# Kernel tuning notes

Hardware: AMD Instinct MI355X
Metric: run time of the kernel (lower is better)

The kernel has to match this reference:

```python
import jax, jax.numpy as jnp
import numpy as np

V, D, S, L, DK, DV, H, B = 32000, 1024, 1024, 4, 64, 64, 16, 4
DFF = 4 * D
EPS = 1e-5


def setup_inputs() -> dict:
    key = jax.random.key(0)
    ks = jax.random.split(key, 20)
    s = 0.02
    n = jax.random.normal
    return {
        "idx": jax.random.randint(ks[0], (B, S), 0, V, dtype=jnp.int32),
        "tok_emb": n(ks[1], (V, D), jnp.float32) * s,
        "pos_emb": n(ks[2], (S, D), jnp.float32) * s,
        "wq": n(ks[3], (L, H, D, DK), jnp.float32) * s,
        "wk": n(ks[4], (L, H, D, DK), jnp.float32) * s,
        "wv": n(ks[5], (L, H, D, DV), jnp.float32) * s,
        "wo": n(ks[6], (L, H * DV, D), jnp.float32) * s,
        "w1": n(ks[7], (L, D, DFF), jnp.float32) * s,
        "b1": jnp.zeros((L, DFF), jnp.float32),
        "w2": n(ks[8], (L, DFF, D), jnp.float32) * s,
        "b2": jnp.zeros((L, D), jnp.float32),
        "ln1_g": jnp.ones((L, D), jnp.float32),
        "ln1_b": jnp.zeros((L, D), jnp.float32),
        "ln2_g": jnp.ones((L, D), jnp.float32),
        "ln2_b": jnp.zeros((L, D), jnp.float32),
        "lnf_g": jnp.ones((D,), jnp.float32),
        "lnf_b": jnp.zeros((D,), jnp.float32),
        "lm_w": n(ks[9], (D, V), jnp.float32) * s,
        "lm_b": jnp.zeros((V,), jnp.float32),
    }


def _ln(x, g, b):
    mu = jnp.mean(x, axis=-1, keepdims=True)
    var = jnp.mean(jnp.square(x - mu), axis=-1, keepdims=True)
    return (x - mu) * jax.lax.rsqrt(var + EPS) * g + b


def _gpt(idx, tok_emb, pos_emb, wq, wk, wv, wo, w1, b1, w2, b2,
         ln1_g, ln1_b, ln2_g, ln2_b, lnf_g, lnf_b, lm_w, lm_b):
    x = tok_emb[idx] + pos_emb[None, :, :]          # [B,S,D]
    causal = jnp.tril(jnp.ones((S, S), bool))        # tril mask buffer
    scale = 1.0 / jnp.sqrt(jnp.asarray(DK, x.dtype))

    def block(x, p):
        wq, wk, wv, wo, w1, b1, w2, b2, g1, be1, g2, be2 = p
        h = _ln(x, g1, be1)
        Q = jnp.einsum('bsd,hdk->bhsk', h, wq)
        K = jnp.einsum('bsd,hdk->bhsk', h, wk)
        Vv = jnp.einsum('bsd,hdv->bhsv', h, wv)
        att = jnp.einsum('bhsk,bhtk->bhst', Q, K) * scale
        att = jnp.where(causal, att, -jnp.inf)
        att = jax.nn.softmax(att, axis=-1)
        o = jnp.einsum('bhst,bhtv->bshv', att, Vv).reshape(x.shape[0], S, H * DV)
        x = x + o @ wo
        h2 = _ln(x, g2, be2)
        x = x + jax.nn.relu(h2 @ w1 + b1) @ w2 + be2 * 0 + b2
        return x, None

    x, _ = jax.lax.scan(block, x, (wq, wk, wv, wo, w1, b1, w2, b2,
                                   ln1_g, ln1_b, ln2_g, ln2_b))
    x = _ln(x, lnf_g, lnf_b)
    logits = x @ lm_w + lm_b                          # [B,S,V]
    return logits


def reference(idx, tok_emb, pos_emb, wq, wk, wv, wo, w1, b1, w2, b2,
              ln1_g, ln1_b, ln2_g, ln2_b, lnf_g, lnf_b, lm_w, lm_b):
    return _gpt(idx, tok_emb, pos_emb, wq, wk, wv, wo, w1, b1, w2, b2,
                ln1_g, ln1_b, ln2_g, ln2_b, lnf_g, lnf_b, lm_w, lm_b)
```

## Files before the change

### kernel.cpp

```cpp
#include <hip/hip_runtime.h>
#include <hip/hip_bf16.h>

#define V_   32000
#define VP_  32768
#define D_   1024
#define S_   1024
#define L_   4
#define H_   16
#define B_   4
#define DFF_ 4096
#define M_   (B_*S_)

using bf_t = __hip_bfloat16;
typedef __bf16 bf16x8 __attribute__((ext_vector_type(8)));
typedef __bf16 bf16x4 __attribute__((ext_vector_type(4)));
typedef float  f32x4  __attribute__((ext_vector_type(4)));

#define AS1(p) ((__attribute__((address_space(1))) void*)(p))
#define AS3(p) ((__attribute__((address_space(3))) void*)(p))

__global__ __launch_bounds__(256) void k_transpose_bf16(
    const float* __restrict__ src, bf_t* __restrict__ dst,
    int R, int C, long srcS1, long srcS2, long dstS1, long dstS2, int n2)
{
  const int z  = blockIdx.z;
  const int z1 = z / n2, z2 = z % n2;
  src += (size_t)z1 * srcS1 + (size_t)z2 * srcS2;
  dst += (size_t)z1 * dstS1 + (size_t)z2 * dstS2;
  __shared__ float tile[32][33];
  const int c0 = blockIdx.x * 32, r0 = blockIdx.y * 32;
  const int lx = threadIdx.x, ly = threadIdx.y;
  #pragma unroll
  for (int i = 0; i < 32; i += 8)
    tile[ly + i][lx] = src[(size_t)(r0 + ly + i) * C + (c0 + lx)];
  __syncthreads();
  #pragma unroll
  for (int i = 0; i < 32; i += 8)
    dst[(size_t)(c0 + ly + i) * R + (r0 + lx)] = __float2bfloat16(tile[lx][ly + i]);
}

__global__ __launch_bounds__(256) void k_embed(
    const int* __restrict__ idx, const float* __restrict__ tok,
    const float* __restrict__ pos, float* __restrict__ x)
{
  const int row = blockIdx.x;
  const int s   = row & (S_ - 1);
  const int t   = idx[row];
  const float4* tr = (const float4*)(tok + (size_t)t * D_);
  const float4* pr = (const float4*)(pos + (size_t)s * D_);
  float4* xr = (float4*)(x + (size_t)row * D_);
  const int i = threadIdx.x;
  float4 a = tr[i], b = pr[i];
  xr[i] = make_float4(a.x + b.x, a.y + b.y, a.z + b.z, a.w + b.w);
}

__global__ __launch_bounds__(256) void k_ln(
    const float* __restrict__ x, const float* __restrict__ g,
    const float* __restrict__ bb, bf_t* __restrict__ out)
{
  __shared__ float red[8];
  const int row = blockIdx.x, tid = threadIdx.x;
  const float4 v = ((const float4*)(x + (size_t)row * D_))[tid];
  float s = v.x + v.y + v.z + v.w;
  #pragma unroll
  for (int o = 32; o > 0; o >>= 1) s += __shfl_down(s, o);
  if ((tid & 63) == 0) red[tid >> 6] = s;
  __syncthreads();
  const float mu = (red[0] + red[1] + red[2] + red[3]) * (1.f / D_);
  const float dx = v.x - mu, dy = v.y - mu, dz = v.z - mu, dw = v.w - mu;
  float ss = dx*dx + dy*dy + dz*dz + dw*dw;
  #pragma unroll
  for (int o = 32; o > 0; o >>= 1) ss += __shfl_down(ss, o);
  if ((tid & 63) == 0) red[4 + (tid >> 6)] = ss;
  __syncthreads();
  const float var = (red[4] + red[5] + red[6] + red[7]) * (1.f / D_);
  const float rs  = rsqrtf(var + 1e-5f);
  const float4 gv = ((const float4*)g)[tid];
  const float4 bv = ((const float4*)bb)[tid];
  const size_t base = (size_t)row * D_ + tid * 4;
  out[base + 0] = __float2bfloat16(dx * rs * gv.x + bv.x);
  out[base + 1] = __float2bfloat16(dy * rs * gv.y + bv.y);
  out[base + 2] = __float2bfloat16(dz * rs * gv.z + bv.z);
  out[base + 3] = __float2bfloat16(dw * rs * gv.w + bv.w);
}

__global__ __launch_bounds__(256) void k_combine_ln(
    float* __restrict__ x, const float* __restrict__ P, long pstride,
    const float* __restrict__ cbias,
    const float* __restrict__ g, const float* __restrict__ bb,
    bf_t* __restrict__ out)
{
  __shared__ float red[8];
  const int row = blockIdx.x, tid = threadIdx.x;
  const size_t i = (size_t)row * 256 + tid;
  float4 a = ((const float4*)x)[i];
  {
    const float4 p0 = ((const float4*)P)[i];
    const float4 p1 = ((const float4*)(P + pstride))[i];
    a.x += p0.x + p1.x; a.y += p0.y + p1.y;
    a.z += p0.z + p1.z; a.w += p0.w + p1.w;
  }
  if (cbias) {
    const float4 bv = ((const float4*)cbias)[tid];
    a.x += bv.x; a.y += bv.y; a.z += bv.z; a.w += bv.w;
  }
  ((float4*)x)[i] = a;
  float s = a.x + a.y + a.z + a.w;
  #pragma unroll
  for (int o = 32; o > 0; o >>= 1) s += __shfl_down(s, o);
  if ((tid & 63) == 0) red[tid >> 6] = s;
  __syncthreads();
  const float mu = (red[0] + red[1] + red[2] + red[3]) * (1.f / D_);
  const float dx = a.x - mu, dy = a.y - mu, dz = a.z - mu, dw = a.w - mu;
  float ss = dx*dx + dy*dy + dz*dz + dw*dw;
  #pragma unroll
  for (int o = 32; o > 0; o >>= 1) ss += __shfl_down(ss, o);
  if ((tid & 63) == 0) red[4 + (tid >> 6)] = ss;
  __syncthreads();
  const float var = (red[4] + red[5] + red[6] + red[7]) * (1.f / D_);
  const float rs  = rsqrtf(var + 1e-5f);
  const float4 gv = ((const float4*)g)[tid];
  const float4 bv = ((const float4*)bb)[tid];
  const size_t base = (size_t)row * D_ + tid * 4;
  out[base + 0] = __float2bfloat16(dx * rs * gv.x + bv.x);
  out[base + 1] = __float2bfloat16(dy * rs * gv.y + bv.y);
  out[base + 2] = __float2bfloat16(dz * rs * gv.z + bv.z);
  out[base + 3] = __float2bfloat16(dw * rs * gv.w + bv.w);
}

template<bool HAS_BIAS, bool RELU, bool OUT_BF16, bool NT, int PARTS>
__global__ __launch_bounds__(256) void k_gemm(
    const bf_t* __restrict__ A, const bf_t* __restrict__ Bt,
    float* outF, bf_t* outB,
    const float* __restrict__ bias,
    int N, int ld, int Klen, long pstride)
{
  __shared__ __bf16 As[128 * 64];
  __shared__ __bf16 Bs[128 * 64];
  const int tid  = threadIdx.x;
  const int lane = tid & 63, wid = tid >> 6;
  int bp = blockIdx.x, kh = 0;
  if (PARTS > 1) { const int T = gridDim.x / PARTS; kh = bp / T; bp %= T; }
  const int i  = bp >> 3;
  const int nt = (bp & 7) + 8 * (i >> 5);
  const int mt = i & 31;
  const int m0 = mt * 128;
  const int n0 = nt * 128;
  if (n0 >= N) return;
  const int kb = kh * Klen;
  f32x4 acc[4][4] = {};

  const int srow = lane >> 3;
  const int scol = (lane & 7) * 8;
  const int mw = (wid >> 1) * 64, nw = (wid & 1) * 64;

  for (int kt = 0; kt < Klen; kt += 64) {
    #pragma unroll
    for (int i2 = 0; i2 < 4; ++i2) {
      const int chunk = i2 * 4 + wid;
      const int r = chunk * 8 + srow;
      const bf_t* sa = A  + (size_t)(m0 + r) * ld + kb + kt + scol;
      const bf_t* sb = Bt + (size_t)(n0 + r) * ld + kb + kt + scol;
      __builtin_amdgcn_global_load_lds(AS1(sa), AS3(&As[chunk * 512]), 16, 0, 0);
      __builtin_amdgcn_global_load_lds(AS1(sb), AS3(&Bs[chunk * 512]), 16, 0, 0);
    }
    asm volatile("s_waitcnt vmcnt(0)" ::: "memory");
    __syncthreads();
    #pragma unroll
    for (int kk = 0; kk < 2; ++kk) {
      bf16x8 af[4], bfr[4];
      #pragma unroll
      for (int mi = 0; mi < 4; ++mi)
        af[mi] = *(const bf16x8*)&As[(mw + mi * 16 + (lane & 15)) * 64 + kk * 32 + (lane >> 4) * 8];
      #pragma unroll
      for (int ni = 0; ni < 4; ++ni)
        bfr[ni] = *(const bf16x8*)&Bs[(nw + ni * 16 + (lane & 15)) * 64 + kk * 32 + (lane >> 4) * 8];
      #pragma unroll
      for (int mi = 0; mi < 4; ++mi)
        #pragma unroll
        for (int ni = 0; ni < 4; ++ni)
          acc[mi][ni] = __builtin_amdgcn_mfma_f32_16x16x32_bf16(af[mi], bfr[ni], acc[mi][ni], 0, 0, 0);
    }
    __syncthreads();
  }

  float* outP = outF + (PARTS > 1 ? (size_t)kh * pstride : 0);
  const int cr = (lane >> 4) * 4, cc = lane & 15;
  #pragma unroll
  for (int mi = 0; mi < 4; ++mi) {
    #pragma unroll
    for (int ni = 0; ni < 4; ++ni) {
      const int col = n0 + nw + ni * 16 + cc;
      const float bv = HAS_BIAS ? bias[col] : 0.f;
      #pragma unroll
      for (int j = 0; j < 4; ++j) {
        const int row = m0 + mw + mi * 16 + cr + j;
        float v = acc[mi][ni][j] + bv;
        if (RELU)  v = fmaxf(v, 0.f);
        if (OUT_BF16) {
          outB[(size_t)row * N + col] = __float2bfloat16(v);
        } else if (NT) {
          __builtin_nontemporal_store(v, &outP[(size_t)row * N + col]);
        } else {
          outP[(size_t)row * N + col] = v;
        }
      }
    }
  }
}

__device__ __forceinline__ void stage256(
    const bf_t* __restrict__ A, const bf_t* __restrict__ Bt,
    int m0, int n0, int lda, int kt, int wid, int lane, __bf16* buf)
{
  #pragma unroll
  for (int p = 0; p < 4; ++p) {
    const int sb   = p * 512 + wid * 64;
    const int slot = sb + lane;
    const int row  = slot >> 3;
    const int c    = (slot & 7) ^ (row & 7);
    __builtin_amdgcn_global_load_lds(AS1(A  + (size_t)(m0 + row) * lda + kt + c * 8),
                                     AS3(buf + sb * 8), 16, 0, 0);
    __builtin_amdgcn_global_load_lds(AS1(Bt + (size_t)(n0 + row) * lda + kt + c * 8),
                                     AS3(buf + 16384 + sb * 8), 16, 0, 0);
  }
}

template<bool HAS_BIAS, bool RELU, bool OUT_BF16, bool NT, int MAP>
__global__ __launch_bounds__(512, 2) void k_gemm256(
    const bf_t* __restrict__ A, const bf_t* __restrict__ Bt,
    float* outF, bf_t* outB, const float* __restrict__ bias,
    int N, int Nvalid, int K)
{
  __shared__ __align__(16) __bf16 LDS[65536];
  const int tid = threadIdx.x, lane = tid & 63, wid = tid >> 6;
  int mt, nt;
  if (MAP == 0) { mt = blockIdx.x & 15; nt = blockIdx.x >> 4; }
  else {
    const int xcd = blockIdx.x & 7, i = blockIdx.x >> 3;
    mt = i & 15; nt = xcd + 8 * (i >> 4);
  }
  const int m0 = mt * 256, n0 = nt * 256;
  if (n0 >= Nvalid) return;
  const int wm = wid >> 2, wn = wid & 3;
  const int l4 = lane & 15, lhi = lane >> 4;

  f32x4 acc[8][4] = {};
  const int NTILES = K >> 6;

  stage256(A, Bt, m0, n0, K, 0,  wid, lane, LDS);
  stage256(A, Bt, m0, n0, K, 64, wid, lane, LDS + 32768);

  for (int t = 0; t < NTILES; ++t) {
    __bf16* buf = LDS + (t & 1) * 32768;
    if (t < NTILES - 1) asm volatile("s_waitcnt vmcnt(8)" ::: "memory");
    else                asm volatile("s_waitcnt vmcnt(0)" ::: "memory");
    __builtin_amdgcn_s_barrier();
    asm volatile("" ::: "memory");
    #pragma unroll
    for (int kk = 0; kk < 2; ++kk) {
      const int ck = kk * 4 + lhi;
      bf16x8 aq[8], bq[4];
      #pragma unroll
      for (int mi = 0; mi < 8; ++mi) {
        const int r = wm * 128 + mi * 16 + l4;
        aq[mi] = *(const bf16x8*)&buf[r * 64 + ((ck ^ (r & 7)) * 8)];
      }
      #pragma unroll
      for (int ni = 0; ni < 4; ++ni) {
        const int r = wn * 64 + ni * 16 + l4;
        bq[ni] = *(const bf16x8*)&buf[16384 + r * 64 + ((ck ^ (r & 7)) * 8)];
      }
      __builtin_amdgcn_s_setprio(1);
      #pragma unroll
      for (int mi = 0; mi < 8; ++mi)
        #pragma unroll
        for (int ni = 0; ni < 4; ++ni)
          acc[mi][ni] = __builtin_amdgcn_mfma_f32_16x16x32_bf16(aq[mi], bq[ni], acc[mi][ni], 0, 0, 0);
      __builtin_amdgcn_s_setprio(0);
    }
    asm volatile("" ::: "memory");
    __builtin_amdgcn_s_barrier();
    if (t + 2 < NTILES)
      stage256(A, Bt, m0, n0, K, (t + 2) * 64, wid, lane, buf);
  }

  float* slab = (float*)LDS + wid * 1088;
  float bval[4];
  if (HAS_BIAS) {
    #pragma unroll
    for (int ni = 0; ni < 4; ++ni) bval[ni] = bias[n0 + wn * 64 + ni * 16 + l4];
  }
  #pragma unroll
  for (int mi = 0; mi < 8; ++mi) {
    #pragma unroll
    for (int ni = 0; ni < 4; ++ni)
      #pragma unroll
      for (int j = 0; j < 4; ++j) {
        float v = acc[mi][ni][j];
        if (HAS_BIAS) v += bval[ni];
        if (RELU) v = fmaxf(v, 0.f);
        slab[(lhi * 4 + j) * 68 + ni * 16 + l4] = v;
      }
    const int grow0 = m0 + wm * 128 + mi * 16;
    const int ncol0 = n0 + wn * 64;
    #pragma unroll
    for (int q = 0; q < 4; ++q) {
      const int r16 = q * 4 + lhi;
      const f32x4 v = *(const f32x4*)&slab[r16 * 68 + l4 * 4];
      const size_t gaddr = (size_t)(grow0 + r16) * N + ncol0 + l4 * 4;
      if (OUT_BF16) {
        bf16x4 o4;
        o4[0] = (__bf16)v[0]; o4[1] = (__bf16)v[1];
        o4[2] = (__bf16)v[2]; o4[3] = (__bf16)v[3];
        *(bf16x4*)(outB + gaddr) = o4;
      } else if (NT) {
        __builtin_nontemporal_store(v, (f32x4*)(outF + gaddr));
      } else {
        *(f32x4*)(outF + gaddr) = v;
      }
    }
  }
}

__global__ __launch_bounds__(256) void k_attn_mfma(
    const bf_t* __restrict__ qkv, bf_t* __restrict__ o)
{
  __shared__ __bf16 Qs[64 * 64];
  __shared__ __bf16 Ks[64 * 64];
  __shared__ __bf16 Vt[64 * 64];
  __shared__ __bf16 Ps[4][16 * 64];

  const int qt = blockIdx.x, bh = blockIdx.y;
  const int b = bh >> 4, h = bh & 15;
  const int tid = threadIdx.x, lane = tid & 63, wid = tid >> 6;
  const int qbase = qt * 64;
  const int r0 = wid * 16;
  const int l4 = lane & 15, lhi = lane >> 4;

  #pragma unroll
  for (int p = 0; p < 2; ++p) {
    const int idx = p * 256 + tid;
    const int r = idx >> 3, c8 = idx & 7;
    const bf16x8 v = *(const bf16x8*)(qkv + (size_t)(b * S_ + qbase + r) * 3072 + h * 64 + c8 * 8);
    *(bf16x8*)&Qs[r * 64 + ((c8 ^ (r & 7)) * 8)] = v;
  }

  f32x4 oa[4];
  #pragma unroll
  for (int di = 0; di < 4; ++di) oa[di] = (f32x4){0.f, 0.f, 0.f, 0.f};
  float mrow = -1e30f, lrow = 0.f;

  const float SCL = 0.125f * 1.44269504089f;

  for (int kt = 0; kt <= qt; ++kt) {
    __syncthreads();
    #pragma unroll
    for (int p = 0; p < 2; ++p) {
      const int idx = p * 256 + tid;
      const int r = idx >> 3, c8 = idx & 7;
      const size_t gbase = (size_t)(b * S_ + kt * 64 + r) * 3072 + h * 64 + c8 * 8;
      const bf16x8 kv = *(const bf16x8*)(qkv + gbase + 1024);
      *(bf16x8*)&Ks[r * 64 + ((c8 ^ (r & 7)) * 8)] = kv;
      const bf16x8 vv = *(const bf16x8*)(qkv + gbase + 2048);
      #pragma unroll
      for (int i = 0; i < 8; ++i) {
        const int d = c8 * 8 + i;
        Vt[d * 64 + (((r >> 3) ^ i ^ c8) * 8) + (r & 7)] = vv[i];
      }
    }
    __syncthreads();

    f32x4 s[4];
    #pragma unroll
    for (int ni = 0; ni < 4; ++ni) s[ni] = (f32x4){0.f, 0.f, 0.f, 0.f};
    const int qr = r0 + l4;
    __builtin_amdgcn_s_setprio(1);
    #pragma unroll
    for (int kk = 0; kk < 2; ++kk) {
      const int ck = kk * 4 + lhi;
      const bf16x8 bq = *(const bf16x8*)&Qs[qr * 64 + ((ck ^ (qr & 7)) * 8)];
      #pragma unroll
      for (int ni = 0; ni < 4; ++ni) {
        const int t = ni * 16 + l4;
        const bf16x8 ak = *(const bf16x8*)&Ks[t * 64 + ((ck ^ (t & 7)) * 8)];
        s[ni] = __builtin_amdgcn_mfma_f32_16x16x32_bf16(ak, bq, s[ni], 0, 0, 0);
      }
    }
    __builtin_amdgcn_s_setprio(0);

    #pragma unroll
    for (int ni = 0; ni < 4; ++ni)
      #pragma unroll
      for (int j = 0; j < 4; ++j)
        s[ni][j] *= SCL;
    if (kt == qt) {
      #pragma unroll
      for (int ni = 0; ni < 4; ++ni)
        #pragma unroll
        for (int j = 0; j < 4; ++j)
          if (ni * 16 + lhi * 4 + j > r0 + l4) s[ni][j] = -1e30f;
    }

    float mloc = -1e30f;
    #pragma unroll
    for (int ni = 0; ni < 4; ++ni)
      #pragma unroll
      for (int j = 0; j < 4; ++j) mloc = fmaxf(mloc, s[ni][j]);
    mloc = fmaxf(mloc, __shfl_xor(mloc, 16));
    mloc = fmaxf(mloc, __shfl_xor(mloc, 32));
    float cscale = 1.f;
    if (!__all(mloc <= mrow + 8.f)) {
      const float mnew = fmaxf(mrow, mloc);
      cscale = exp2f(mrow - mnew);
      #pragma unroll
      for (int j = 0; j < 4; ++j) {
        const float cj = __shfl(cscale, lhi * 4 + j);
        #pragma unroll
        for (int di = 0; di < 4; ++di) oa[di][j] *= cj;
      }
      mrow = mnew;
    }
    float ssum = 0.f;
    #pragma unroll
    for (int ni = 0; ni < 4; ++ni)
      #pragma unroll
      for (int j = 0; j < 4; ++j) {
        const float pv = exp2f(s[ni][j] - mrow);
        s[ni][j] = pv;
        ssum += pv;
      }
    ssum += __shfl_xor(ssum, 16);
    ssum += __shfl_xor(ssum, 32);
    lrow = lrow * cscale + ssum;

    #pragma unroll
    for (int ni = 0; ni < 4; ++ni)
      #pragma unroll
      for (int j = 0; j < 4; ++j) {
        const int c = ni * 16 + lhi * 4 + j;
        Ps[wid][l4 * 64 + (((c >> 3) ^ (l4 & 7)) * 8) + (c & 7)] = (__bf16)s[ni][j];
      }

    __builtin_amdgcn_s_setprio(1);
    #pragma unroll
    for (int kk = 0; kk < 2; ++kk) {
      const int ck = kk * 4 + lhi;
      const bf16x8 ap = *(const bf16x8*)&Ps[wid][l4 * 64 + ((ck ^ (l4 & 7)) * 8)];
      #pragma unroll
      for (int di = 0; di < 4; ++di) {
        const int d = di * 16 + l4;
        const bf16x8 bv = *(const bf16x8*)&Vt[d * 64 + ((ck ^ (d & 7) ^ ((d >> 3) & 7)) * 8)];
        oa[di] = __builtin_amdgcn_mfma_f32_16x16x32_bf16(ap, bv, oa[di], 0, 0, 0);
      }
    }
    __builtin_amdgcn_s_setprio(0);
  }

  #pragma unroll
  for (int j = 0; j < 4; ++j) {
    const float lj = __shfl(lrow, lhi * 4 + j);
    const float inv = 1.f / lj;
    const size_t row = (size_t)(b * S_) + qbase + r0 + lhi * 4 + j;
    #pragma unroll
    for (int di = 0; di < 4; ++di)
      o[row * 1024 + h * 64 + di * 16 + l4] = __float2bfloat16(oa[di][j] * inv);
  }
}

extern "C" void kernel_launch(void* const* d_in, const int* in_sizes, int n_in,
                              void* d_out, int out_size, void* d_ws, size_t ws_size,
                              hipStream_t stream)
{
  (void)in_sizes; (void)n_in; (void)out_size; (void)ws_size;
  const int*   idx  = (const int*)  d_in[0];
  const float* tok  = (const float*)d_in[1];
  const float* pos  = (const float*)d_in[2];
  const float* wq   = (const float*)d_in[3];
  const float* wk   = (const float*)d_in[4];
  const float* wv   = (const float*)d_in[5];
  const float* wo   = (const float*)d_in[6];
  const float* w1   = (const float*)d_in[7];
  const float* b1   = (const float*)d_in[8];
  const float* w2   = (const float*)d_in[9];
  const float* b2   = (const float*)d_in[10];
  const float* ln1g = (const float*)d_in[11];
  const float* ln1b = (const float*)d_in[12];
  const float* ln2g = (const float*)d_in[13];
  const float* ln2b = (const float*)d_in[14];
  const float* lnfg = (const float*)d_in[15];
  const float* lnfb = (const float*)d_in[16];
  const float* lmw  = (const float*)d_in[17];
  const float* lmb  = (const float*)d_in[18];
  float* out = (float*)d_out;

  char* ws = (char*)d_ws;
  size_t off = 0;
  auto alloc = [&](size_t bytes) {
    void* p = ws + off; off += (bytes + 255) & ~(size_t)255; return p;
  };
  bf_t*  qkvw = (bf_t*) alloc((size_t)L_ * 3072 * 1024 * 2);
  bf_t*  wot  = (bf_t*) alloc((size_t)L_ * 1024 * 1024 * 2);
  bf_t*  w1t  = (bf_t*) alloc((size_t)L_ * 4096 * 1024 * 2);
  bf_t*  w2t  = (bf_t*) alloc((size_t)L_ * 1024 * 4096 * 2);
  bf_t*  lmwt = (bf_t*) alloc((size_t)VP_ * 1024 * 2);
  float* x    = (float*)alloc((size_t)M_ * D_ * 4);
  bf_t*  hbuf = (bf_t*) alloc((size_t)M_ * D_ * 2);
  bf_t*  qkvb = (bf_t*) alloc((size_t)M_ * 3072 * 2);
  bf_t*  attb = (bf_t*) alloc((size_t)M_ * D_ * 2);
  bf_t*  ffnb = (bf_t*) alloc((size_t)M_ * DFF_ * 2);
  float* PpartO = (float*)ffnb;
  float* PpartF = (float*)qkvb;
  const long PSTRIDE = (long)M_ * 1024;

  const dim3 tb(32, 8);
  k_transpose_bf16<<<dim3(2, 32, L_*H_), tb, 0, stream>>>(
      wq, qkvw + 0 * 1024 * 1024, D_, 64,
      (long)H_*D_*64, (long)D_*64, (long)3*1024*1024, (long)64*1024, H_);
  k_transpose_bf16<<<dim3(2, 32, L_*H_), tb, 0, stream>>>(
      wk, qkvw + 1 * 1024 * 1024, D_, 64,
      (long)H_*D_*64, (long)D_*64, (long)3*1024*1024, (long)64*1024, H_);
  k_transpose_bf16<<<dim3(2, 32, L_*H_), tb, 0, stream>>>(
      wv, qkvw + 2 * 1024 * 1024, D_, 64,
      (long)H_*D_*64, (long)D_*64, (long)3*1024*1024, (long)64*1024, H_);
  k_transpose_bf16<<<dim3(32, 32, L_), tb, 0, stream>>>(
      wo, wot, 1024, 1024, (long)1024*1024, 0, (long)1024*1024, 0, 1);
  k_transpose_bf16<<<dim3(128, 32, L_), tb, 0, stream>>>(
      w1, w1t, 1024, 4096, (long)1024*4096, 0, (long)1024*4096, 0, 1);
  k_transpose_bf16<<<dim3(32, 128, L_), tb, 0, stream>>>(
      w2, w2t, 4096, 1024, (long)4096*1024, 0, (long)4096*1024, 0, 1);
  k_transpose_bf16<<<dim3(1000, 32, 1), tb, 0, stream>>>(
      lmw, lmwt, 1024, V_, 0, 0, 0, 0, 1);

  k_embed<<<M_, 256, 0, stream>>>(idx, tok, pos, x);
  k_ln<<<M_, 256, 0, stream>>>(x, ln1g, ln1b, hbuf);

  for (int l = 0; l < L_; ++l) {
    k_gemm256<false, false, true, false, 0><<<12 * 16, 512, 0, stream>>>(
        hbuf, qkvw + (size_t)l * 3072 * 1024, nullptr, qkvb, nullptr,
        3072, 3072, 1024);
    k_attn_mfma<<<dim3(S_ / 64, B_ * H_), 256, 0, stream>>>(qkvb, attb);
    k_gemm<false, false, false, false, 2><<<2 * 8 * 32, 256, 0, stream>>>(
        attb, wot + (size_t)l * 1024 * 1024, PpartO, nullptr, nullptr,
        1024, 1024, 512, PSTRIDE);
    k_combine_ln<<<M_, 256, 0, stream>>>(
        x, PpartO, PSTRIDE, nullptr, ln2g + l * D_, ln2b + l * D_, hbuf);
    k_gemm256<true, true, true, false, 0><<<16 * 16, 512, 0, stream>>>(
        hbuf, w1t + (size_t)l * 4096 * 1024, nullptr, ffnb, b1 + l * DFF_,
        4096, 4096, 1024);
    k_gemm<false, false, false, false, 2><<<2 * 8 * 32, 256, 0, stream>>>(
        ffnb, w2t + (size_t)l * 1024 * 4096, PpartF, nullptr, nullptr,
        1024, 4096, 2048, PSTRIDE);
    const float* ng = (l < L_ - 1) ? (ln1g + (l + 1) * D_) : lnfg;
    const float* nb = (l < L_ - 1) ? (ln1b + (l + 1) * D_) : lnfb;
    k_combine_ln<<<M_, 256, 0, stream>>>(
        x, PpartF, PSTRIDE, b2 + l * D_, ng, nb, hbuf);
  }

  k_gemm256<true, false, false, true, 1><<<16 * 128, 512, 0, stream>>>(
      hbuf, lmwt, out, nullptr, lmb,
      V_, V_, 1024);
}
```

Baseline: 1.424 ms.

## Swizzle LDS in 128-tile GEMM and overlap next-tile staging with MFMAs

The 128x128 GEMM now stores and reads its LDS tiles with an XOR swizzle on the 16-byte chunk index, to cut bank conflicts on the fragment reads. In the 256x256 GEMM, both k-halves of fragments are read from LDS up front. The first half of the MFMAs runs, then the barrier is taken and the global-to-LDS staging for tile t+2 is issued, and the second half of the MFMAs runs while those loads are in flight. This hides load-issue latency behind compute. In exchange, the doubled fragment registers (aq0/aq1, bq0/bq1) raise VGPR pressure, which may limit occupancy.

```diff
diff --git a/kernel.cpp b/kernel.cpp
--- a/kernel.cpp
+++ b/kernel.cpp
@@ -151,7 +151,7 @@
   f32x4 acc[4][4] = {};
 
   const int srow = lane >> 3;
-  const int scol = (lane & 7) * 8;
+  const int scol = ((lane & 7) ^ (lane >> 3)) * 8;
   const int mw = (wid >> 1) * 64, nw = (wid & 1) * 64;
 
   for (int kt = 0; kt < Klen; kt += 64) {
@@ -168,13 +168,18 @@
     __syncthreads();
     #pragma unroll
     for (int kk = 0; kk < 2; ++kk) {
+      const int ck = kk * 4 + (lane >> 4);
       bf16x8 af[4], bfr[4];
       #pragma unroll
-      for (int mi = 0; mi < 4; ++mi)
-        af[mi] = *(const bf16x8*)&As[(mw + mi * 16 + (lane & 15)) * 64 + kk * 32 + (lane >> 4) * 8];
-      #pragma unroll
-      for (int ni = 0; ni < 4; ++ni)
-        bfr[ni] = *(const bf16x8*)&Bs[(nw + ni * 16 + (lane & 15)) * 64 + kk * 32 + (lane >> 4) * 8];
+      for (int mi = 0; mi < 4; ++mi) {
+        const int r = mw + mi * 16 + (lane & 15);
+        af[mi] = *(const bf16x8*)&As[r * 64 + ((ck ^ (r & 7)) * 8)];
+      }
+      #pragma unroll
+      for (int ni = 0; ni < 4; ++ni) {
+        const int r = nw + ni * 16 + (lane & 15);
+        bfr[ni] = *(const bf16x8*)&Bs[r * 64 + ((ck ^ (r & 7)) * 8)];
+      }
       #pragma unroll
       for (int mi = 0; mi < 4; ++mi)
         #pragma unroll
@@ -257,32 +262,40 @@
     else                asm volatile("s_waitcnt vmcnt(0)" ::: "memory");
     __builtin_amdgcn_s_barrier();
     asm volatile("" ::: "memory");
-    #pragma unroll
-    for (int kk = 0; kk < 2; ++kk) {
-      const int ck = kk * 4 + lhi;
-      bf16x8 aq[8], bq[4];
-      #pragma unroll
-      for (int mi = 0; mi < 8; ++mi) {
-        const int r = wm * 128 + mi * 16 + l4;
-        aq[mi] = *(const bf16x8*)&buf[r * 64 + ((ck ^ (r & 7)) * 8)];
-      }
-      #pragma unroll
-      for (int ni = 0; ni < 4; ++ni) {
-        const int r = wn * 64 + ni * 16 + l4;
-        bq[ni] = *(const bf16x8*)&buf[16384 + r * 64 + ((ck ^ (r & 7)) * 8)];
-      }
-      __builtin_amdgcn_s_setprio(1);
-      #pragma unroll
-      for (int mi = 0; mi < 8; ++mi)
-        #pragma unroll
-        for (int ni = 0; ni < 4; ++ni)
-          acc[mi][ni] = __builtin_amdgcn_mfma_f32_16x16x32_bf16(aq[mi], bq[ni], acc[mi][ni], 0, 0, 0);
-      __builtin_amdgcn_s_setprio(0);
-    }
-    asm volatile("" ::: "memory");
+    const int ck0 = lhi, ck1 = 4 + lhi;
+    bf16x8 aq0[8], aq1[8], bq0[4], bq1[4];
+    #pragma unroll
+    for (int mi = 0; mi < 8; ++mi) {
+      const int r = wm * 128 + mi * 16 + l4;
+      aq0[mi] = *(const bf16x8*)&buf[r * 64 + ((ck0 ^ (r & 7)) * 8)];
+      aq1[mi] = *(const bf16x8*)&buf[r * 64 + ((ck1 ^ (r & 7)) * 8)];
+    }
+    #pragma unroll
+    for (int ni = 0; ni < 4; ++ni) {
+      const int r = wn * 64 + ni * 16 + l4;
+      bq0[ni] = *(const bf16x8*)&buf[16384 + r * 64 + ((ck0 ^ (r & 7)) * 8)];
+      bq1[ni] = *(const bf16x8*)&buf[16384 + r * 64 + ((ck1 ^ (r & 7)) * 8)];
+    }
+    __builtin_amdgcn_s_setprio(1);
+    #pragma unroll
+    for (int mi = 0; mi < 8; ++mi)
+      #pragma unroll
+      for (int ni = 0; ni < 4; ++ni)
+        acc[mi][ni] = __builtin_amdgcn_mfma_f32_16x16x32_bf16(aq0[mi], bq0[ni], acc[mi][ni], 0, 0, 0);
+    __builtin_amdgcn_s_setprio(0);
+    asm volatile("s_waitcnt lgkmcnt(0)" ::: "memory");
+    __builtin_amdgcn_sched_barrier(0);
     __builtin_amdgcn_s_barrier();
     if (t + 2 < NTILES)
       stage256(A, Bt, m0, n0, K, (t + 2) * 64, wid, lane, buf);
+    __builtin_amdgcn_s_setprio(1);
+    #pragma unroll
+    for (int mi = 0; mi < 8; ++mi)
+      #pragma unroll
+      for (int ni = 0; ni < 4; ++ni)
+        acc[mi][ni] = __builtin_amdgcn_mfma_f32_16x16x32_bf16(aq1[mi], bq1[ni], acc[mi][ni], 0, 0, 0);
+    __builtin_amdgcn_s_setprio(0);
+    asm volatile("" ::: "memory");
   }
 
   float* slab = (float*)LDS + wid * 1088;
```

Result: faster. 1.350 ms (-5.2%).
